# Optimization experiments

Measured on AMD Instinct MI355X. Metric: run time of the kernel, lower is better.

## Reference

```python
import jax, jax.numpy as jnp
import numpy as np

E, H, V, ENC, ATT, P, B, T = 512, 512, 32000, 2048, 512, 196, 64, 20


def setup_inputs() -> dict:
    key = jax.random.key(0)
    ks = jax.random.split(key, 24)
    s = 0.02
    inp = {
        "encoder_out": jax.random.normal(ks[0], (B, P, ENC), jnp.float32),
        "captions": jax.random.randint(ks[1], (B, T), 0, V),
        "lengths": T,
        "emb": jax.random.normal(ks[2], (V, E), jnp.float32) * s,
        "Wea": jax.random.normal(ks[3], (ENC, ATT), jnp.float32) * s,
        "bea": jnp.zeros((ATT,), jnp.float32),
        "Wda": jax.random.normal(ks[4], (H, ATT), jnp.float32) * s,
        "bda": jnp.zeros((ATT,), jnp.float32),
        "Wfa": jax.random.normal(ks[5], (ATT, 1), jnp.float32) * s,
        "bfa": jnp.zeros((1,), jnp.float32),
        "W_ih0": jax.random.normal(ks[6], (4 * H, E + ENC), jnp.float32) * s,
        "W_hh0": jax.random.normal(ks[7], (4 * H, H), jnp.float32) * s,
        "b_ih0": jnp.zeros((4 * H,), jnp.float32),
        "b_hh0": jnp.zeros((4 * H,), jnp.float32),
        "W_ih1": jax.random.normal(ks[8], (4 * H, H), jnp.float32) * s,
        "W_hh1": jax.random.normal(ks[9], (4 * H, H), jnp.float32) * s,
        "b_ih1": jnp.zeros((4 * H,), jnp.float32),
        "b_hh1": jnp.zeros((4 * H,), jnp.float32),
        "Wfc": jax.random.normal(ks[10], (H, V), jnp.float32) * s,
        "bfc": jnp.zeros((V,), jnp.float32),
        "Wih": jax.random.normal(ks[11], (ENC, H), jnp.float32) * s,
        "bih": jnp.zeros((H,), jnp.float32),
        "Wic": jax.random.normal(ks[12], (ENC, H), jnp.float32) * s,
        "bic": jnp.zeros((H,), jnp.float32),
    }
    return inp


def _lstm_cell(x, h, c, W_ih, W_hh, b_ih, b_hh):
    # PyTorch gate order: i, f, g, o
    g = x @ W_ih.T + b_ih + h @ W_hh.T + b_hh
    i, f, gg, o = jnp.split(g, 4, axis=-1)
    c_new = jax.nn.sigmoid(f) * c + jax.nn.sigmoid(i) * jnp.tanh(gg)
    h_new = jax.nn.sigmoid(o) * jnp.tanh(c_new)
    return h_new, c_new


def reference(encoder_out, captions, lengths, emb, Wea, bea, Wda, bda, Wfa, bfa,
              W_ih0, W_hh0, b_ih0, b_hh0, W_ih1, W_hh1, b_ih1, b_hh1,
              Wfc, bfc, Wih, bih, Wic, bic):
    # init hidden state from mean pooled encoder output, repeated over layers
    mean_enc = encoder_out.mean(axis=1)                  # [B, ENC]
    h0 = mean_enc @ Wih + bih                            # [B, H]
    c0 = mean_enc @ Wic + bic
    h = jnp.stack([h0, h0])                              # [2, B, H]
    c = jnp.stack([c0, c0])

    att1 = encoder_out @ Wea + bea                       # [B, P, ATT] (constant across t)
    embs = jnp.take(emb, captions, axis=0)               # [B, T, E]
    embs_t = jnp.swapaxes(embs, 0, 1)                    # [T, B, E]

    def step(carry, emb_t):
        h, c = carry
        hid = h[-1]                                      # top-layer hidden [B, H]
        att2 = hid @ Wda + bda                           # [B, ATT]
        e = (jax.nn.relu(att1 + att2[:, None, :]) @ Wfa + bfa)[..., 0]  # [B, P]
        alpha = jax.nn.softmax(e, axis=1)
        awe = jnp.einsum('bp,bpd->bd', alpha, encoder_out)              # [B, ENC]
        x = jnp.concatenate([emb_t, awe], axis=1)        # [B, E+ENC]
        h0n, c0n = _lstm_cell(x, h[0], c[0], W_ih0, W_hh0, b_ih0, b_hh0)
        h1n, c1n = _lstm_cell(h0n, h[1], c[1], W_ih1, W_hh1, b_ih1, b_hh1)
        pred = h1n @ Wfc + bfc                           # [B, V] (dropout = identity in eval)
        return (jnp.stack([h0n, h1n]), jnp.stack([c0n, c1n])), pred

    _, preds = jax.lax.scan(step, (h, c), embs_t[:lengths])
    return jnp.swapaxes(preds, 0, 1)                     # [B, T, V]
```

## Files before the change

### kernel.cpp

```cpp
#include <hip/hip_runtime.h>

#define ENCD 2048
#define ATTD 512
#define HIDD 512
#define NB 64
#define NP 196
#define NT 20
#define NV 32000
#define NE 512

using s8v = __attribute__((ext_vector_type(8))) short;
using f4v = __attribute__((ext_vector_type(4))) float;
#define MFMA_B16 __builtin_amdgcn_mfma_f32_16x16x32_bf16

__device__ inline short f2b(float f) {
  union { float f; unsigned u; } v; v.f = f;
  unsigned r = v.u + 0x7fff + ((v.u >> 16) & 1);
  return (short)(r >> 16);
}
__device__ inline float b2f(short s) {
  union { unsigned u; float f; } v; v.u = ((unsigned)(unsigned short)s) << 16;
  return v.f;
}

__global__ void conv_mean(const float* __restrict__ enc, short* __restrict__ encB,
                          short* __restrict__ meB) {
  int b = blockIdx.x >> 2, kq = blockIdx.x & 3;
  int k = kq * 512 + threadIdx.x * 2;
  const float* src = enc + (size_t)b * NP * ENCD + k;
  short* dst = encB + (size_t)b * NP * ENCD + k;
  float a0 = 0.f, a1 = 0.f;
  for (int p = 0; p < NP; ++p) {
    float2 v = *(const float2*)(src + (size_t)p * ENCD);
    a0 += v.x; a1 += v.y;
    short2 o; o.x = f2b(v.x); o.y = f2b(v.y);
    *(short2*)(dst + (size_t)p * ENCD) = o;
  }
  short2 m; m.x = f2b(a0 * (1.f / NP)); m.y = f2b(a1 * (1.f / NP));
  *(short2*)(meB + (size_t)b * ENCD + k) = m;
}

__global__ void emb_b16(const int* __restrict__ caps, const float* __restrict__ emb,
                        short* __restrict__ embB) {
  int t = blockIdx.x / NB, b = blockIdx.x % NB;
  int cap = caps[b * NT + t];
  int k = threadIdx.x;
  for (int r = 0; r < 2; ++r, k += 256)
    embB[((size_t)t * NB + b) * NE + k] = f2b(emb[(size_t)cap * NE + k]);
}

__global__ void swz_rm(const float* __restrict__ B, int N, short* __restrict__ dst) {
  __shared__ short lt[256 * 32];
  int tid = threadIdx.x;
  int k0 = blockIdx.x * 32, n0 = blockIdx.y * 256;
  for (int k = 0; k < 32; ++k)
    lt[tid * 32 + k] = f2b(B[(size_t)(k0 + k) * N + n0 + tid]);
  __syncthreads();
  int NT16 = N >> 4;
  for (int r = 0; r < 4; ++r) {
    int idx = r * 256 + tid;
    int lane = idx & 63, ntl = idx >> 6;
    int srcn = ntl * 16 + (lane & 15), srck = (lane >> 4) * 8;
    short* o = dst + ((size_t)blockIdx.x * NT16 + (n0 >> 4) + ntl) * 512 + lane * 8;
    for (int i = 0; i < 8; ++i) o[i] = lt[srcn * 32 + srck + i];
  }
}

__global__ void swz_lstm(const float* __restrict__ Wih, int Kih, const float* __restrict__ Whh,
                         short* __restrict__ dst) {
  int tid = threadIdx.x, lane = tid & 63;
  int ct = blockIdx.y * 4 + (tid >> 6);
  int n = ct * 16 + (lane & 15);
  int k = blockIdx.x * 32 + ((lane >> 4) << 3);
  short* o = dst + ((size_t)blockIdx.x * 128 + ct) * 512 + lane * 8;
  for (int i = 0; i < 8; ++i) {
    int kk = k + i;
    float f = (kk < Kih) ? Wih[(size_t)n * Kih + kk] : Whh[(size_t)n * 512 + (kk - Kih)];
    o[i] = f2b(f);
  }
}

__global__ void bias_sum(const float* __restrict__ a, const float* __restrict__ b,
                         float* __restrict__ o, int n) {
  int i = blockIdx.x * 256 + threadIdx.x;
  if (i < n) o[i] = a[i] + b[i];
}

__global__ void __launch_bounds__(256) att1_tiled(
    const short* __restrict__ A, const short* __restrict__ Bs,
    const float* __restrict__ bias, short* __restrict__ att1B) {
  __shared__ short as[2][64][40];
  int tid = threadIdx.x, lane = tid & 63, w = tid >> 6;
  int m0 = blockIdx.x * 64;
  int mrow = lane & 15, kq = lane >> 4;
  int sr = tid >> 2, sc = (tid & 3) * 8;
  f4v acc[4][8] = {};
  *(s8v*)&as[0][sr][sc] = *(const s8v*)(A + (size_t)(m0 + sr) * 2048 + sc);
  __syncthreads();
  for (int ks = 0; ks < 64; ++ks) {
    int cur = ks & 1;
    if (ks < 63)
      *(s8v*)&as[cur ^ 1][sr][sc] = *(const s8v*)(A + (size_t)(m0 + sr) * 2048 + (ks + 1) * 32 + sc);
    s8v a[4], b[8];
#pragma unroll
    for (int mi = 0; mi < 4; ++mi)
      a[mi] = *(const s8v*)&as[cur][mi * 16 + mrow][kq * 8];
#pragma unroll
    for (int ni = 0; ni < 8; ++ni)
      b[ni] = *(const s8v*)(Bs + ((size_t)ks * 32 + w * 8 + ni) * 512 + lane * 8);
#pragma unroll
    for (int mi = 0; mi < 4; ++mi)
#pragma unroll
      for (int ni = 0; ni < 8; ++ni)
        acc[mi][ni] = MFMA_B16(a[mi], b[ni], acc[mi][ni], 0, 0, 0);
    __syncthreads();
  }
#pragma unroll
  for (int mi = 0; mi < 4; ++mi)
#pragma unroll
    for (int ni = 0; ni < 8; ++ni) {
      int col = (w * 8 + ni) * 16 + mrow;
      int rbase = m0 + mi * 16 + kq * 4;
      float bv = bias[col];
      for (int r = 0; r < 4; ++r)
        att1B[(size_t)(rbase + r) * 512 + col] = f2b(acc[mi][ni][r] + bv);
    }
}

__global__ void init_mfma(const short* __restrict__ A,
                          const short* __restrict__ BsH, const short* __restrict__ BsC,
                          const float* __restrict__ bih, const float* __restrict__ bic,
                          short* __restrict__ h0, short* __restrict__ h1,
                          float* __restrict__ c0v, float* __restrict__ c1v) {
  int lane = threadIdx.x & 63;
  int mi = blockIdx.x, jt0 = blockIdx.y;
  bool isC = jt0 >= 32;
  int jt = jt0 & 31;
  const short* Bs = isC ? BsC : BsH;
  int mrow = lane & 15, kq = lane >> 4;
  f4v acc = {};
  const short* aBase = A + (size_t)(mi * 16 + mrow) * 2048 + kq * 8;
  const short* bBase = Bs + lane * 8;
#pragma unroll 4
  for (int ks = 0; ks < 64; ++ks) {
    s8v a = *(const s8v*)(aBase + ks * 32);
    s8v b = *(const s8v*)(bBase + ((size_t)ks * 32 + jt) * 512);
    acc = MFMA_B16(a, b, acc, 0, 0, 0);
  }
  int j = jt * 16 + mrow;
  float bv = (isC ? bic : bih)[j];
  for (int r = 0; r < 4; ++r) {
    int b = mi * 16 + kq * 4 + r;
    size_t idx = (size_t)b * 512 + j;
    float o = acc[r] + bv;
    if (isC) { c0v[idx] = o; c1v[idx] = o; }
    else     { short s = f2b(o); h0[idx] = s; h1[idx] = s; }
  }
}

template<int KSEG, int KBASE>
__device__ __forceinline__ void seg_mm(const short* __restrict__ aRow, int kh, int kq,
                                       int ct, const short* __restrict__ bBase, f4v& acc) {
  constexpr int HALF = KSEG / 2;
  const int kl0 = kh * HALF;
#pragma unroll 4
  for (int i = 0; i < HALF / 32; ++i) {
    int kl = kl0 + i * 32;
    s8v a = *(const s8v*)(aRow + kl + kq * 8);
    int ksi = (KBASE + kl) >> 5;
    s8v b = *(const s8v*)(bBase + ((size_t)ksi * 128 + ct) * 512);
    acc = MFMA_B16(a, b, acc, 0, 0, 0);
  }
}

template<int K1, int K2, int K3>
__global__ void __launch_bounds__(512) lstm_t(
    const short* __restrict__ A1, const short* __restrict__ A2,
    const short* __restrict__ A3,
    const short* __restrict__ Bs, const float* __restrict__ bias,
    float* __restrict__ c_st, short* __restrict__ h_out) {
  __shared__ f4v gsh[8][64];
  int tid = threadIdx.x, lane = tid & 63, w = tid >> 6;
  int g = w >> 1, kh = w & 1;
  int jt = blockIdx.x, mi = blockIdx.y;
  int mrow = lane & 15, kq = lane >> 4;
  int m = mi * 16 + mrow;
  int ct = g * 32 + jt;
  f4v acc = {};
  const short* bBase = Bs + lane * 8;
  seg_mm<K1, 0>(A1 + (size_t)m * K1, kh, kq, ct, bBase, acc);
  seg_mm<K2, K1>(A2 + (size_t)m * K2, kh, kq, ct, bBase, acc);
  if constexpr (K3 > 0)
    seg_mm<K3, K1 + K2>(A3 + (size_t)m * K3, kh, kq, ct, bBase, acc);
  gsh[w][lane] = acc;
  __syncthreads();
  if (tid < 256) {
    int b_l = tid >> 4, j_l = tid & 15;
    int lsrc = (b_l >> 2) * 16 + j_l, r = b_l & 3;
    int j = jt * 16 + j_l;
    float ii = gsh[0][lsrc][r] + gsh[1][lsrc][r] + bias[j];
    float ff = gsh[2][lsrc][r] + gsh[3][lsrc][r] + bias[512 + j];
    float gg = gsh[4][lsrc][r] + gsh[5][lsrc][r] + bias[1024 + j];
    float oo = gsh[6][lsrc][r] + gsh[7][lsrc][r] + bias[1536 + j];
    size_t idx = (size_t)(mi * 16 + b_l) * 512 + j;
    float c_old = c_st[idx];
    float si = 1.f / (1.f + expf(-ii));
    float sf = 1.f / (1.f + expf(-ff));
    float so = 1.f / (1.f + expf(-oo));
    float cn = sf * c_old + si * tanhf(gg);
    c_st[idx] = cn;
    h_out[idx] = f2b(so * tanhf(cn));
  }
}

__global__ void att2_mfma(const short* __restrict__ A, const short* __restrict__ Bs,
                          const float* __restrict__ bias, float* __restrict__ C) {
  int tid = threadIdx.x, lane = tid & 63, mi = tid >> 6;
  int nt = blockIdx.x;
  int mrow = lane & 15, kq = lane >> 4;
  f4v acc = {};
  const short* aBase = A + (size_t)(mi * 16 + mrow) * 512 + kq * 8;
  const short* bBase = Bs + lane * 8;
#pragma unroll
  for (int ks = 0; ks < 16; ++ks) {
    s8v a = *(const s8v*)(aBase + ks * 32);
    s8v b = *(const s8v*)(bBase + ((size_t)ks * 32 + nt) * 512);
    acc = MFMA_B16(a, b, acc, 0, 0, 0);
  }
  int col = nt * 16 + mrow;
  float bv = bias[col];
  for (int r = 0; r < 4; ++r) C[(size_t)(mi * 16 + kq * 4 + r) * 512 + col] = acc[r] + bv;
}

__global__ void esc_kernel(const short* __restrict__ att1B, const float* __restrict__ att2,
                           const float* __restrict__ Wfa, const float* __restrict__ bfa,
                           float* __restrict__ eG) {
  int b = blockIdx.x >> 2, pq = blockIdx.x & 3;
  int tid = threadIdx.x, lane = tid & 63, w = tid >> 6;
  float a2[8], wf[8];
  const float* a2p = att2 + b * 512 + lane * 8;
  const float* wfp = Wfa + lane * 8;
#pragma unroll
  for (int i = 0; i < 8; ++i) { a2[i] = a2p[i]; wf[i] = wfp[i]; }
  float bf0 = bfa[0];
  int p0 = pq * 49;
  for (int p = p0 + w; p < p0 + 49; p += 4) {
    s8v av = *(const s8v*)(att1B + ((size_t)b * NP + p) * 512 + lane * 8);
    float acc = 0.f;
#pragma unroll
    for (int i = 0; i < 8; ++i) {
      float v = b2f(av[i]) + a2[i];
      acc += fmaxf(v, 0.f) * wf[i];
    }
    for (int off = 32; off; off >>= 1) acc += __shfl_xor(acc, off, 64);
    if (lane == 0) eG[b * 256 + p] = acc + bf0;
  }
}

__global__ void smax_awe(const float* __restrict__ eG, const short* __restrict__ encB,
                         short* __restrict__ aweB) {
  __shared__ float red[256];
  __shared__ float alpha[256];
  int b = blockIdx.x >> 2, dq = blockIdx.x & 3, tid = threadIdx.x;
  float e = (tid < NP) ? eG[b * 256 + tid] : -1e30f;
  red[tid] = e; __syncthreads();
  for (int s = 128; s; s >>= 1) { if (tid < s) red[tid] = fmaxf(red[tid], red[tid + s]); __syncthreads(); }
  float mx = red[0]; __syncthreads();
  float ex = (tid < NP) ? expf(e - mx) : 0.f;
  red[tid] = ex; __syncthreads();
  for (int s = 128; s; s >>= 1) { if (tid < s) red[tid] += red[tid + s]; __syncthreads(); }
  float inv = 1.f / red[0];
  alpha[tid] = ex * inv;
  __syncthreads();
  int d = dq * 512 + tid * 2;
  const short* base = encB + (size_t)b * NP * ENCD + d;
  float a0 = 0.f, a1 = 0.f;
#pragma unroll 7
  for (int p = 0; p < NP; ++p) {
    short2 vv = *(const short2*)(base + (size_t)p * ENCD);
    float a = alpha[p];
    a0 += a * b2f(vv.x); a1 += a * b2f(vv.y);
  }
  short2 o; o.x = f2b(a0); o.y = f2b(a1);
  *(short2*)(aweB + (size_t)b * ENCD + d) = o;
}

__global__ void __launch_bounds__(512) predseq_mfma(
    const short* __restrict__ A,
    const short* __restrict__ Bs,
    const float* __restrict__ bias,
    float* __restrict__ out) {
  __shared__ short bls[16][8][64 * 8];
  int tid = threadIdx.x, lane = tid & 63, wid = tid >> 6;
  int ntg = blockIdx.x * 8;
  int mt0 = blockIdx.y * 10;
  int mrow = lane & 15, kq = lane >> 4;
#pragma unroll
  for (int it = 0; it < 16; ++it) {
    int ei = it * 512 + tid;
    int ks = ei >> 9, rem = ei & 511;
    int ni = rem >> 6, ln = rem & 63;
    *(s8v*)&bls[ks][ni][ln * 8] = *(const s8v*)(Bs + ((size_t)ks * 2000 + ntg + ni) * 512 + ln * 8);
  }
  __syncthreads();
  for (int mt = mt0 + wid; mt < mt0 + 10; mt += 8) {
    int m0 = mt * 64;
    f4v acc[4][8] = {};
    const short* aBase = A + (size_t)(m0 + mrow) * 512 + kq * 8;
#pragma unroll 2
    for (int ks = 0; ks < 16; ++ks) {
      s8v a[4], b[8];
#pragma unroll
      for (int mi = 0; mi < 4; ++mi) a[mi] = *(const s8v*)(aBase + mi * 16 * 512 + ks * 32);
#pragma unroll
      for (int ni = 0; ni < 8; ++ni) b[ni] = *(const s8v*)&bls[ks][ni][lane * 8];
#pragma unroll
      for (int mi = 0; mi < 4; ++mi)
#pragma unroll
        for (int ni = 0; ni < 8; ++ni)
          acc[mi][ni] = MFMA_B16(b[ni], a[mi], acc[mi][ni], 0, 0, 0);
    }
#pragma unroll
    for (int ni = 0; ni < 8; ++ni) {
      int v0 = (ntg + ni) * 16 + kq * 4;
      float4 bv4 = *(const float4*)&bias[v0];
#pragma unroll
      for (int mi = 0; mi < 4; ++mi) {
        int row = m0 + mi * 16 + mrow;
        int bb = row & 63, t = row >> 6;
        float4 o4;
        o4.x = acc[mi][ni][0] + bv4.x;
        o4.y = acc[mi][ni][1] + bv4.y;
        o4.z = acc[mi][ni][2] + bv4.z;
        o4.w = acc[mi][ni][3] + bv4.w;
        *(float4*)&out[((size_t)bb * NT + t) * NV + v0] = o4;
      }
    }
  }
}

extern "C" void kernel_launch(void* const* d_in, const int* in_sizes, int n_in,
                              void* d_out, int out_size, void* d_ws, size_t ws_size,
                              hipStream_t stream) {
  const float* enc   = (const float*)d_in[0];
  const int*   caps  = (const int*)d_in[1];
  const float* emb   = (const float*)d_in[3];
  const float* Wea   = (const float*)d_in[4];
  const float* bea   = (const float*)d_in[5];
  const float* Wda   = (const float*)d_in[6];
  const float* bda   = (const float*)d_in[7];
  const float* Wfa   = (const float*)d_in[8];
  const float* bfa   = (const float*)d_in[9];
  const float* W_ih0 = (const float*)d_in[10];
  const float* W_hh0 = (const float*)d_in[11];
  const float* b_ih0 = (const float*)d_in[12];
  const float* b_hh0 = (const float*)d_in[13];
  const float* W_ih1 = (const float*)d_in[14];
  const float* W_hh1 = (const float*)d_in[15];
  const float* b_ih1 = (const float*)d_in[16];
  const float* b_hh1 = (const float*)d_in[17];
  const float* Wfc   = (const float*)d_in[18];
  const float* bfc   = (const float*)d_in[19];
  const float* Wih   = (const float*)d_in[20];
  const float* bih   = (const float*)d_in[21];
  const float* Wic   = (const float*)d_in[22];
  const float* bic   = (const float*)d_in[23];
  float* out = (float*)d_out;

  char* cw = (char*)d_ws;
  auto alloc = [&](size_t bytes) { char* p = cw; cw += (bytes + 255) & ~(size_t)255; return p; };
  short* encB  = (short*)alloc((size_t)12544 * 2048 * 2);
  short* att1B = (short*)alloc((size_t)12544 * 512 * 2);
  short* embB  = (short*)alloc((size_t)NT * NB * NE * 2);
  short* WeaS  = (short*)alloc((size_t)2048 * 512 * 2);
  short* WdaS  = (short*)alloc((size_t)512 * 512 * 2);
  short* WfcS  = (short*)alloc((size_t)512 * 32000 * 2);
  short* Wl0S  = (short*)alloc((size_t)3072 * 2048 * 2);
  short* Wl1S  = (short*)alloc((size_t)1024 * 2048 * 2);
  short* WihS  = (short*)alloc((size_t)2048 * 512 * 2);
  short* WicS  = (short*)alloc((size_t)2048 * 512 * 2);
  short* meB   = (short*)alloc((size_t)64 * 2048 * 2);
  float* bsum0 = (float*)alloc(2048 * 4);
  float* bsum1 = (float*)alloc(2048 * 4);
  float* att2  = (float*)alloc((size_t)64 * 512 * 4);
  float* eG    = (float*)alloc((size_t)64 * 256 * 4);
  short* h0b[2] = { (short*)alloc(64 * 512 * 2), (short*)alloc(64 * 512 * 2) };
  short* h1init = (short*)alloc(64 * 512 * 2);
  short* h1seq  = (short*)alloc((size_t)NT * 64 * 512 * 2);
  float* c0 = (float*)alloc(64 * 512 * 4);
  float* c1 = (float*)alloc(64 * 512 * 4);
  short* aweB = (short*)alloc((size_t)64 * 2048 * 2);

  conv_mean<<<256, 256, 0, stream>>>(enc, encB, meB);
  emb_b16<<<NT * NB, 256, 0, stream>>>(caps, emb, embB);
  swz_rm<<<dim3(64, 2), 256, 0, stream>>>(Wea, 512, WeaS);
  swz_rm<<<dim3(16, 2), 256, 0, stream>>>(Wda, 512, WdaS);
  swz_rm<<<dim3(16, 125), 256, 0, stream>>>(Wfc, 32000, WfcS);
  swz_rm<<<dim3(64, 2), 256, 0, stream>>>(Wih, 512, WihS);
  swz_rm<<<dim3(64, 2), 256, 0, stream>>>(Wic, 512, WicS);
  swz_lstm<<<dim3(96, 32), 256, 0, stream>>>(W_ih0, 2560, W_hh0, Wl0S);
  swz_lstm<<<dim3(32, 32), 256, 0, stream>>>(W_ih1, 512, W_hh1, Wl1S);
  bias_sum<<<8, 256, 0, stream>>>(b_ih0, b_hh0, bsum0, 2048);
  bias_sum<<<8, 256, 0, stream>>>(b_ih1, b_hh1, bsum1, 2048);
  att1_tiled<<<196, 256, 0, stream>>>(encB, WeaS, bea, att1B);
  init_mfma<<<dim3(4, 64), 64, 0, stream>>>(meB, WihS, WicS, bih, bic,
                                            h0b[0], h1init, c0, c1);

  const short* h1prev = h1init;
  int cur = 0;
  for (int t = 0; t < NT; ++t) {
    int nxt = cur ^ 1;
    att2_mfma<<<32, 256, 0, stream>>>(h1prev, WdaS, bda, att2);
    esc_kernel<<<NB * 4, 256, 0, stream>>>(att1B, att2, Wfa, bfa, eG);
    smax_awe<<<NB * 4, 256, 0, stream>>>(eG, encB, aweB);
    lstm_t<512, 2048, 512><<<dim3(32, 4), 512, 0, stream>>>(
        embB + (size_t)t * NB * NE, aweB, h0b[cur],
        Wl0S, bsum0, c0, h0b[nxt]);
    short* h1out = h1seq + (size_t)t * NB * HIDD;
    lstm_t<512, 512, 0><<<dim3(32, 4), 512, 0, stream>>>(
        h0b[nxt], h1prev, nullptr,
        Wl1S, bsum1, c1, h1out);
    h1prev = h1out;
    cur = nxt;
  }
  predseq_mfma<<<dim3(250, 2), 512, 0, stream>>>(h1seq, WfcS, bfc, out);
}
```

Measured before the change: 1.357 ms.

## Merge setup launches and halve predseq N-tile for more blocks

Two swizzle launches for Wih/Wic are merged into one kernel indexed by blockIdx.z, and two bias-sum launches are merged into one, cutting launch count. The final vocab projection kernel now covers 4 N-tiles per block instead of 8, doubling the grid to 1000 blocks and halving LDS and accumulator registers per block to raise occupancy. The trade-off is that each A tile is read from global memory twice as often, and the inner loop unroll goes from 2 to 4.

Measured after the change: 1.376 ms. No clear change (+1.4%).

```diff
diff --git a/kernel.cpp b/kernel.cpp
--- a/kernel.cpp
+++ b/kernel.cpp
@@ -66,6 +66,25 @@
   }
 }
 
+__global__ void swz_rm2(const float* __restrict__ B0, short* __restrict__ D0,
+                        const float* __restrict__ B1, short* __restrict__ D1) {
+  __shared__ short lt[256 * 32];
+  const float* B = blockIdx.z ? B1 : B0;
+  short* dst = blockIdx.z ? D1 : D0;
+  int tid = threadIdx.x;
+  int k0 = blockIdx.x * 32, n0 = blockIdx.y * 256;
+  for (int k = 0; k < 32; ++k)
+    lt[tid * 32 + k] = f2b(B[(size_t)(k0 + k) * 512 + n0 + tid]);
+  __syncthreads();
+  for (int r = 0; r < 4; ++r) {
+    int idx = r * 256 + tid;
+    int lane = idx & 63, ntl = idx >> 6;
+    int srcn = ntl * 16 + (lane & 15), srck = (lane >> 4) * 8;
+    short* o = dst + ((size_t)blockIdx.x * 32 + (n0 >> 4) + ntl) * 512 + lane * 8;
+    for (int i = 0; i < 8; ++i) o[i] = lt[srcn * 32 + srck + i];
+  }
+}
+
 __global__ void swz_lstm(const float* __restrict__ Wih, int Kih, const float* __restrict__ Whh,
                          short* __restrict__ dst) {
   int tid = threadIdx.x, lane = tid & 63;
@@ -80,10 +99,13 @@
   }
 }
 
-__global__ void bias_sum(const float* __restrict__ a, const float* __restrict__ b,
-                         float* __restrict__ o, int n) {
-  int i = blockIdx.x * 256 + threadIdx.x;
-  if (i < n) o[i] = a[i] + b[i];
+__global__ void bias_sum2(const float* __restrict__ a0, const float* __restrict__ b0,
+                          float* __restrict__ o0,
+                          const float* __restrict__ a1, const float* __restrict__ b1,
+                          float* __restrict__ o1) {
+  int i = (blockIdx.x & 7) * 256 + threadIdx.x;
+  if (blockIdx.x < 8) o0[i] = a0[i] + b0[i];
+  else                o1[i] = a1[i] + b1[i];
 }
 
 __global__ void __launch_bounds__(256) att1_tiled(
@@ -290,38 +312,38 @@
     const short* __restrict__ Bs,
     const float* __restrict__ bias,
     float* __restrict__ out) {
-  __shared__ short bls[16][8][64 * 8];
+  __shared__ short bls[16][4][64 * 8];
   int tid = threadIdx.x, lane = tid & 63, wid = tid >> 6;
-  int ntg = blockIdx.x * 8;
+  int ntg = blockIdx.x * 4;
   int mt0 = blockIdx.y * 10;
   int mrow = lane & 15, kq = lane >> 4;
 #pragma unroll
-  for (int it = 0; it < 16; ++it) {
+  for (int it = 0; it < 8; ++it) {
     int ei = it * 512 + tid;
-    int ks = ei >> 9, rem = ei & 511;
+    int ks = ei >> 8, rem = ei & 255;
     int ni = rem >> 6, ln = rem & 63;
     *(s8v*)&bls[ks][ni][ln * 8] = *(const s8v*)(Bs + ((size_t)ks * 2000 + ntg + ni) * 512 + ln * 8);
   }
   __syncthreads();
   for (int mt = mt0 + wid; mt < mt0 + 10; mt += 8) {
     int m0 = mt * 64;
-    f4v acc[4][8] = {};
+    f4v acc[4][4] = {};
     const short* aBase = A + (size_t)(m0 + mrow) * 512 + kq * 8;
-#pragma unroll 2
+#pragma unroll 4
     for (int ks = 0; ks < 16; ++ks) {
-      s8v a[4], b[8];
+      s8v a[4], b[4];
 #pragma unroll
       for (int mi = 0; mi < 4; ++mi) a[mi] = *(const s8v*)(aBase + mi * 16 * 512 + ks * 32);
 #pragma unroll
-      for (int ni = 0; ni < 8; ++ni) b[ni] = *(const s8v*)&bls[ks][ni][lane * 8];
+      for (int ni = 0; ni < 4; ++ni) b[ni] = *(const s8v*)&bls[ks][ni][lane * 8];
 #pragma unroll
       for (int mi = 0; mi < 4; ++mi)
 #pragma unroll
-        for (int ni = 0; ni < 8; ++ni)
+        for (int ni = 0; ni < 4; ++ni)
           acc[mi][ni] = MFMA_B16(b[ni], a[mi], acc[mi][ni], 0, 0, 0);
     }
 #pragma unroll
-    for (int ni = 0; ni < 8; ++ni) {
+    for (int ni = 0; ni < 4; ++ni) {
       int v0 = (ntg + ni) * 16 + kq * 4;
       float4 bv4 = *(const float4*)&bias[v0];
 #pragma unroll
@@ -396,12 +418,10 @@
   swz_rm<<<dim3(64, 2), 256, 0, stream>>>(Wea, 512, WeaS);
   swz_rm<<<dim3(16, 2), 256, 0, stream>>>(Wda, 512, WdaS);
   swz_rm<<<dim3(16, 125), 256, 0, stream>>>(Wfc, 32000, WfcS);
-  swz_rm<<<dim3(64, 2), 256, 0, stream>>>(Wih, 512, WihS);
-  swz_rm<<<dim3(64, 2), 256, 0, stream>>>(Wic, 512, WicS);
+  swz_rm2<<<dim3(64, 2, 2), 256, 0, stream>>>(Wih, WihS, Wic, WicS);
   swz_lstm<<<dim3(96, 32), 256, 0, stream>>>(W_ih0, 2560, W_hh0, Wl0S);
   swz_lstm<<<dim3(32, 32), 256, 0, stream>>>(W_ih1, 512, W_hh1, Wl1S);
-  bias_sum<<<8, 256, 0, stream>>>(b_ih0, b_hh0, bsum0, 2048);
-  bias_sum<<<8, 256, 0, stream>>>(b_ih1, b_hh1, bsum1, 2048);
+  bias_sum2<<<16, 256, 0, stream>>>(b_ih0, b_hh0, bsum0, b_ih1, b_hh1, bsum1);
   att1_tiled<<<196, 256, 0, stream>>>(encB, WeaS, bea, att1B);
   init_mfma<<<dim3(4, 64), 64, 0, stream>>>(meB, WihS, WicS, bih, bic,
                                             h0b[0], h1init, c0, c1);
@@ -423,5 +443,5 @@
     h1prev = h1out;
     cur = nxt;
   }
-  predseq_mfma<<<dim3(250, 2), 512, 0, stream>>>(h1seq, WfcS, bfc, out);
-}
+  predseq_mfma<<<dim3(500, 2), 512, 0, stream>>>(h1seq, WfcS, bfc, out);
+}
```
